# Kernel tuning notes

Measured on AMD Instinct MI355X. Metric: run time of the kernel, lower is better.

Reference implementation:

```python
import jax, jax.numpy as jnp
import numpy as np

B, S, D = 4, 4096, 1024  # batch, seq_len, input_dim == key_dim == value_dim == output_dim


def setup_inputs() -> dict:
    key = jax.random.key(0)
    kx, kq, kk, kv, kp = jax.random.split(key, 5)
    scale = 1.0 / np.sqrt(D)
    return {
        "x": jax.random.normal(kx, (B, S, D), dtype=jnp.float32),
        # weights stored as (in_dim, out_dim) so projection is x @ W
        "Wq": jax.random.normal(kq, (D, D), dtype=jnp.float32) * scale,
        "Wk": jax.random.normal(kk, (D, D), dtype=jnp.float32) * scale,
        "Wv": jax.random.normal(kv, (D, D), dtype=jnp.float32) * scale,
        "P": jax.random.normal(kp, (D, D), dtype=jnp.float32) * scale,
    }


def reference(x, Wq, Wk, Wv, P):
    # Linear (softmax-free) self-attention, faithful to the torch module:
    # Q K^T then (.)V, materializing the (B,S,S) score matrix as the original does.
    Q = jnp.einsum("bsd,dk->bsk", x, Wq)
    K = jnp.einsum("bsd,dk->bsk", x, Wk)
    V = jnp.einsum("bsd,dv->bsv", x, Wv)
    scores = jnp.einsum("bsk,btk->bst", Q, K)   # (B,S,S)
    context = jnp.einsum("bst,btv->bsv", scores, V)
    return x + jnp.einsum("bsv,vo->bso", context, P)
```

## Files before the change

### kernel.cpp

```cpp
#include <hip/hip_runtime.h>
#include <hip/hip_bf16.h>
#include <stdint.h>


#define BATCH 4
#define SEQ   4096
#define DIM   1024

#define TRI_SLICE 589824l

typedef __bf16 bf16x8 __attribute__((ext_vector_type(8)));
typedef float f32x4 __attribute__((ext_vector_type(4)));

static __device__ __forceinline__ unsigned short f2bf(float f) {
    unsigned int u = __builtin_bit_cast(unsigned int, f);
    u += 0x7fff + ((u >> 16) & 1);
    return (unsigned short)(u >> 16);
}
static __device__ __forceinline__ float bf2f(unsigned short h) {
    unsigned int u = (unsigned int)h << 16;
    return __builtin_bit_cast(float, u);
}

__global__ __launch_bounds__(256)
void gemm_fin(const unsigned short* __restrict__ Ag,
              const unsigned short* __restrict__ Btg,
              float* __restrict__ Cg,
              int K, int lda, int ldbt, int ldc,
              long sA, long sBt, long sC)
{
    __shared__ unsigned short As[3][128][32];
    __shared__ unsigned short Bs[3][256][32];

    const int gx = gridDim.x, gy = gridDim.y;
    const int nwg = gx * gy * gridDim.z;
    int id = blockIdx.x + gx * (blockIdx.y + gy * blockIdx.z);
    id = (id & 7) * (nwg >> 3) + (id >> 3);

    const int bx = id % gx;
    const int rest = id / gx;
    const int by = rest % gy;
    const int b = rest / gy;
    const long i0 = (long)by * 128;
    const long j0 = (long)bx * 256;

    const unsigned short* A  = Ag  + (long)b * sA;
    const unsigned short* Bt = Btg + (long)b * sBt;

    const int tid  = threadIdx.x;
    const int lane = tid & 63;
    const int w    = tid >> 6;
    const int wr   = w >> 1, wc = w & 1;
    const int srow = lane >> 2;
    const int sch  = lane & 3;
    const int fr   = lane & 15;
    const int kg   = lane >> 4;
    const int ch   = (kg ^ ((fr >> 1) & 3)) * 8;

    f32x4 acc[4][8] = {};
    const int nt = K / 32;

    auto stage = [&](int t, int buf) {
        const long kk = (long)t * 32;
        const long scoff = (long)((sch ^ ((srow >> 1) & 3)) * 8);
#pragma unroll
        for (int inst = 0; inst < 2; ++inst) {
            const int row = inst * 64 + w * 16 + srow;
            const unsigned short* src = A + (i0 + row) * lda + kk + scoff;
            __builtin_amdgcn_global_load_lds(
                (const __attribute__((address_space(1))) void*)src,
                (__attribute__((address_space(3))) void*)&As[buf][inst * 64 + w * 16][0],
                16, 0, 0);
        }
#pragma unroll
        for (int inst = 0; inst < 4; ++inst) {
            const int row = inst * 64 + w * 16 + srow;
            const unsigned short* src = Bt + (j0 + row) * ldbt + kk + scoff;
            __builtin_amdgcn_global_load_lds(
                (const __attribute__((address_space(1))) void*)src,
                (__attribute__((address_space(3))) void*)&Bs[buf][inst * 64 + w * 16][0],
                16, 0, 0);
        }
    };

    stage(0, 0);
    stage(1, 1);
    stage(2, 2);

    for (int t = 0; t < nt; ++t) {
        const int buf = t % 3;
        if (t < nt - 2)       asm volatile("s_waitcnt vmcnt(12)" ::: "memory");
        else if (t == nt - 2) asm volatile("s_waitcnt vmcnt(6)" ::: "memory");
        else                  asm volatile("s_waitcnt vmcnt(0)" ::: "memory");
        __builtin_amdgcn_s_barrier();
        asm volatile("" ::: "memory");

        bf16x8 af[4], bfv[8];
#pragma unroll
        for (int m = 0; m < 4; ++m)
            af[m] = *(const bf16x8*)&As[buf][wr * 64 + m * 16 + fr][ch];
#pragma unroll
        for (int n = 0; n < 8; ++n)
            bfv[n] = *(const bf16x8*)&Bs[buf][wc * 128 + n * 16 + fr][ch];

        asm volatile("s_waitcnt lgkmcnt(0)" ::: "memory");
        __builtin_amdgcn_sched_barrier(0);
        __builtin_amdgcn_s_barrier();
        asm volatile("" ::: "memory");

        if (t + 3 < nt) stage(t + 3, buf);
        __builtin_amdgcn_sched_barrier(0);

        __builtin_amdgcn_s_setprio(1);
#pragma unroll
        for (int m = 0; m < 4; ++m)
#pragma unroll
            for (int n = 0; n < 8; ++n)
                acc[m][n] = __builtin_amdgcn_mfma_f32_16x16x32_bf16(
                    af[m], bfv[n], acc[m][n], 0, 0, 0);
        __builtin_amdgcn_s_setprio(0);
    }

    float* C32 = Cg + (long)b * sC;
#pragma unroll
    for (int m = 0; m < 4; ++m) {
        const long rbase = i0 + wr * 64 + m * 16 + kg * 4;
#pragma unroll
        for (int n = 0; n < 8; ++n) {
            const long col = j0 + wc * 128 + n * 16 + fr;
#pragma unroll
            for (int q = 0; q < 4; ++q)
                C32[(rbase + q) * ldc + col] = acc[m][n][q];
        }
    }
}

template<int OUTMODE, int BN, bool TRI, bool ADD_I>
__global__ __launch_bounds__(256)
void gemm_db(const unsigned short* __restrict__ Ag,
             const unsigned short* __restrict__ Btg,
             void* __restrict__ Cg,
             int K, int zdiv, int lda, int ldbt, int ldc,
             long sA, long sBt, long sC)
{
    constexpr int NF = BN / 32;
    __shared__ unsigned short As[2][128][64];
    __shared__ unsigned short Bs[2][BN][64];

    const int gx = gridDim.x, gy = gridDim.y;
    const int nwg = gx * gy * gridDim.z;
    int id = blockIdx.x + gx * (blockIdx.y + gy * blockIdx.z);
    id = (id & 7) * (nwg >> 3) + (id >> 3);

    int z, tlin = 0;
    long i0, j0;
    if (TRI) {
        z = id / 36;
        tlin = id % 36;
        int t = tlin, ti = 0;
        while (t > ti) { t -= ti + 1; ++ti; }
        i0 = (long)ti * 128;
        j0 = (long)t * 128;
    } else {
        const int bx = id % gx;
        const int rest = id / gx;
        const int by = rest % gy;
        z = rest / gy;
        i0 = (long)by * 128;
        j0 = (long)bx * BN;
    }
    const int b = z / zdiv;
    const long koff = (long)(z % zdiv) * K;

    const unsigned short* A  = Ag  + (long)b * sA  + koff;
    const unsigned short* Bt = Btg + (long)b * sBt + koff;

    const int tid  = threadIdx.x;
    const int lane = tid & 63;
    const int w    = tid >> 6;
    const int wr   = w >> 1, wc = w & 1;
    const int lrow = lane >> 3;
    const int lcol = lane & 7;
    const int fr   = lane & 15;
    const int kg   = lane >> 4;
    const int scol = (lcol ^ lrow) * 8;

    f32x4 acc[4][NF] = {};

    const int nt = K / 64;

    auto stage = [&](int t, int buf) {
        const long kk = (long)t * 64;
#pragma unroll
        for (int inst = 0; inst < 4; ++inst) {
            const int row = w * 32 + inst * 8;
            const unsigned short* srcA = A + (i0 + row + lrow) * lda + kk + scol;
            __builtin_amdgcn_global_load_lds(
                (const __attribute__((address_space(1))) void*)srcA,
                (__attribute__((address_space(3))) void*)&As[buf][row][0], 16, 0, 0);
        }
#pragma unroll
        for (int inst = 0; inst < NF; ++inst) {
            const int row = w * (8 * NF) + inst * 8;
            const unsigned short* srcB = Bt + (j0 + row + lrow) * ldbt + kk + scol;
            __builtin_amdgcn_global_load_lds(
                (const __attribute__((address_space(1))) void*)srcB,
                (__attribute__((address_space(3))) void*)&Bs[buf][row][0], 16, 0, 0);
        }
    };

    stage(0, 0);
    stage(1, 1);

    for (int t = 0; t < nt; ++t) {
        const int buf = t & 1;
        if (t < nt - 1) {
            if constexpr (BN == 128)
                asm volatile("s_waitcnt vmcnt(8)" ::: "memory");
            else
                asm volatile("s_waitcnt vmcnt(6)" ::: "memory");
        } else {
            asm volatile("s_waitcnt vmcnt(0)" ::: "memory");
        }
        __builtin_amdgcn_s_barrier();
        asm volatile("" ::: "memory");

        bf16x8 af0[4], bf0[NF], af1[4], bf1[NF];
        const int ch0 = (kg ^ (fr & 7)) * 8;
        const int ch1 = ((4 + kg) ^ (fr & 7)) * 8;
#pragma unroll
        for (int m = 0; m < 4; ++m)
            af0[m] = *(const bf16x8*)&As[buf][wr * 64 + m * 16 + fr][ch0];
#pragma unroll
        for (int n = 0; n < NF; ++n)
            bf0[n] = *(const bf16x8*)&Bs[buf][wc * (BN / 2) + n * 16 + fr][ch0];
#pragma unroll
        for (int m = 0; m < 4; ++m)
            af1[m] = *(const bf16x8*)&As[buf][wr * 64 + m * 16 + fr][ch1];
#pragma unroll
        for (int n = 0; n < NF; ++n)
            bf1[n] = *(const bf16x8*)&Bs[buf][wc * (BN / 2) + n * 16 + fr][ch1];

        __builtin_amdgcn_s_setprio(1);
#pragma unroll
        for (int m = 0; m < 4; ++m)
#pragma unroll
            for (int n = 0; n < NF; ++n)
                acc[m][n] = __builtin_amdgcn_mfma_f32_16x16x32_bf16(
                    af0[m], bf0[n], acc[m][n], 0, 0, 0);
        __builtin_amdgcn_s_setprio(0);

        asm volatile("s_waitcnt lgkmcnt(0)" ::: "memory");
        __builtin_amdgcn_sched_barrier(0);
        __builtin_amdgcn_s_barrier();
        asm volatile("" ::: "memory");

        if (t + 2 < nt) stage(t + 2, buf);
        __builtin_amdgcn_sched_barrier(0);

        __builtin_amdgcn_s_setprio(1);
#pragma unroll
        for (int m = 0; m < 4; ++m)
#pragma unroll
            for (int n = 0; n < NF; ++n)
                acc[m][n] = __builtin_amdgcn_mfma_f32_16x16x32_bf16(
                    af1[m], bf1[n], acc[m][n], 0, 0, 0);
        __builtin_amdgcn_s_setprio(0);
    }

    if (OUTMODE == 3) {
        unsigned short* Cp = (unsigned short*)Cg + (long)z * TRI_SLICE
                           + (long)tlin * 16384;
#pragma unroll
        for (int m = 0; m < 4; ++m) {
            const int lrb = wr * 64 + m * 16 + kg * 4;
#pragma unroll
            for (int n = 0; n < NF; ++n) {
                const int lc = wc * (BN / 2) + n * 16 + fr;
#pragma unroll
                for (int q = 0; q < 4; ++q)
                    Cp[(lrb + q) * 128 + lc] = f2bf(acc[m][n][q]);
            }
        }
        return;
    }

    unsigned short* C16 = (OUTMODE == 1) ? ((unsigned short*)Cg + (long)b * sC) : nullptr;
    float*          C32 = (OUTMODE == 0) ? ((float*)Cg + (long)b * sC) : nullptr;
#pragma unroll
    for (int m = 0; m < 4; ++m) {
        const long rbase = i0 + wr * 64 + m * 16 + kg * 4;
#pragma unroll
        for (int n = 0; n < NF; ++n) {
            const long col = j0 + wc * (BN / 2) + n * 16 + fr;
#pragma unroll
            for (int q = 0; q < 4; ++q) {
                const long r = rbase + q;
                float v = acc[m][n][q];
                if (ADD_I && r == col) v += 1.0f;
                if (OUTMODE == 1) C16[r * ldc + col] = f2bf(v);
                else              C32[r * ldc + col] = v;
            }
        }
    }
}

__global__ __launch_bounds__(256)
void reduce_cast_tri(const unsigned short* __restrict__ part,
                     unsigned short* __restrict__ outG, int split)
{
    __shared__ unsigned short s[8][132];
    const long DD = (long)DIM * DIM;
    int id = blockIdx.x * 256 + threadIdx.x;
    const int b  = id / 147456;
    int rem      = id % 147456;
    const int tlin = rem / 4096;
    const int rr = rem % 4096;
    const int r  = rr >> 5;
    const int c4 = rr & 31;
    int t = tlin, ti = 0;
    while (t > ti) { t -= ti + 1; ++ti; }
    const long off = (long)tlin * 16384 + r * 128 + c4 * 4;

    float4 sum = make_float4(0.f, 0.f, 0.f, 0.f);
    for (int sp = 0; sp < split; ++sp) {
        ushort4 v = *(const ushort4*)&part[(long)(b * split + sp) * TRI_SLICE + off];
        sum.x += bf2f(v.x); sum.y += bf2f(v.y); sum.z += bf2f(v.z); sum.w += bf2f(v.w);
    }
    ushort4 o;
    o.x = f2bf(sum.x); o.y = f2bf(sum.y); o.z = f2bf(sum.z); o.w = f2bf(sum.w);
    *(ushort4*)&outG[b * DD + ((long)ti * 128 + r) * DIM + (long)t * 128 + c4 * 4] = o;

    if (t == ti) return;

    const int rl = r & 7;
    s[rl][c4 * 4 + 0] = o.x; s[rl][c4 * 4 + 1] = o.y;
    s[rl][c4 * 4 + 2] = o.z; s[rl][c4 * 4 + 3] = o.w;
    __syncthreads();

    const int r0 = r & ~7;
    const int co = threadIdx.x >> 1;
    const int hf = threadIdx.x & 1;
    ushort4 m;
    m.x = s[hf * 4 + 0][co]; m.y = s[hf * 4 + 1][co];
    m.z = s[hf * 4 + 2][co]; m.w = s[hf * 4 + 3][co];
    *(ushort4*)&outG[b * DD + ((long)t * 128 + co) * DIM
                     + (long)ti * 128 + r0 + hf * 4] = m;
}

__global__ __launch_bounds__(256)
void prep_all(const float* __restrict__ x,
              const float* __restrict__ Wq, const float* __restrict__ Wk,
              const float* __restrict__ Wv, const float* __restrict__ P,
              unsigned short* __restrict__ xb, unsigned short* __restrict__ xTb,
              unsigned short* __restrict__ Wqb, unsigned short* __restrict__ Wkb,
              unsigned short* __restrict__ Wvb, unsigned short* __restrict__ Ptb)
{
    __shared__ unsigned short t[32][33];
    const int z = blockIdx.z;
    const int row = threadIdx.x >> 3;
    const int cid = threadIdx.x & 7;

    if (z < BATCH) {
        const long base = (long)z * SEQ * DIM;
        const int r0 = blockIdx.y * 32;
        const int c0 = blockIdx.x * 32;
        float4 v = *(const float4*)&x[base + (long)(r0 + row) * DIM + c0 + cid * 4];
        ushort4 h;
        h.x = f2bf(v.x); h.y = f2bf(v.y); h.z = f2bf(v.z); h.w = f2bf(v.w);
        *(ushort4*)&xb[base + (long)(r0 + row) * DIM + c0 + cid * 4] = h;
        t[row][cid * 4 + 0] = h.x; t[row][cid * 4 + 1] = h.y;
        t[row][cid * 4 + 2] = h.z; t[row][cid * 4 + 3] = h.w;
        __syncthreads();
        ushort4 o;
        o.x = t[cid * 4 + 0][row];
        o.y = t[cid * 4 + 1][row];
        o.z = t[cid * 4 + 2][row];
        o.w = t[cid * 4 + 3][row];
        *(ushort4*)&xTb[base + (long)(c0 + row) * SEQ + r0 + cid * 4] = o;
        return;
    }

    const int wsel = blockIdx.y >> 5;
    const int r0 = (blockIdx.y & 31) * 32;
    const int c0 = blockIdx.x * 32;
    const float* src = (wsel == 0) ? Wq : (wsel == 1) ? Wk : (wsel == 2) ? Wv : P;
    float4 v = *(const float4*)&src[(long)(r0 + row) * DIM + c0 + cid * 4];
    ushort4 h;
    h.x = f2bf(v.x); h.y = f2bf(v.y); h.z = f2bf(v.z); h.w = f2bf(v.w);

    if (wsel < 3) {
        unsigned short* dst = (wsel == 0) ? Wqb : (wsel == 1) ? Wkb : Wvb;
        *(ushort4*)&dst[(long)(r0 + row) * DIM + c0 + cid * 4] = h;
        return;
    }
    t[row][cid * 4 + 0] = h.x; t[row][cid * 4 + 1] = h.y;
    t[row][cid * 4 + 2] = h.z; t[row][cid * 4 + 3] = h.w;
    __syncthreads();
    ushort4 o;
    o.x = t[cid * 4 + 0][row];
    o.y = t[cid * 4 + 1][row];
    o.z = t[cid * 4 + 2][row];
    o.w = t[cid * 4 + 3][row];
    *(ushort4*)&Ptb[(long)(c0 + row) * DIM + r0 + cid * 4] = o;
}

extern "C" void kernel_launch(void* const* d_in, const int* in_sizes, int n_in,
                              void* d_out, int out_size, void* d_ws, size_t ws_size,
                              hipStream_t stream)
{
    const float* x  = (const float*)d_in[0];
    const float* Wq = (const float*)d_in[1];
    const float* Wk = (const float*)d_in[2];
    const float* Wv = (const float*)d_in[3];
    const float* P  = (const float*)d_in[4];
    float* out = (float*)d_out;

    const long DD = (long)DIM * DIM;
    const long SD = (long)SEQ * DIM;

    uint8_t* ws = (uint8_t*)d_ws;
    unsigned short* xb   = (unsigned short*)(ws);
    unsigned short* xTb  = (unsigned short*)(ws + (32ul << 20));
    unsigned short* Hb   = (unsigned short*)(ws + (32ul << 20));
    unsigned short* Ntb  = (unsigned short*)(ws + (40ul << 20));
    unsigned short* Gb   = (unsigned short*)(ws + (64ul << 20));
    unsigned short* Wqb  = (unsigned short*)(ws + (72ul << 20));
    unsigned short* Ptb  = (unsigned short*)(ws + (74ul << 20));
    unsigned short* Wkb  = (unsigned short*)(ws + (76ul << 20));
    unsigned short* Wvb  = (unsigned short*)(ws + (78ul << 20));
    unsigned short* Ub   = (unsigned short*)(ws + (80ul << 20));
    unsigned short* W2Tb = (unsigned short*)(ws + (82ul << 20));
    unsigned short* regA = (unsigned short*)(ws + (84ul << 20));

    const int split = 8;

    prep_all<<<dim3(DIM / 32, SEQ / 32, BATCH + 1), 256, 0, stream>>>(
        x, Wq, Wk, Wv, P, xb, xTb, Wqb, Wkb, Wvb, Ptb);

    gemm_db<3, 128, true, false><<<dim3(36 * split * BATCH, 1, 1), 256, 0, stream>>>(
        xTb, xTb, regA, SEQ / split, split, SEQ, SEQ, DIM, SD, SD, 0);
    reduce_cast_tri<<<dim3(BATCH * 36 * 128 * 32 / 256), 256, 0, stream>>>(
        regA, Gb, split);

    gemm_db<1, 64, false, false><<<dim3(16, 8, 2), 256, 0, stream>>>(
        Wqb, Wkb, Ub, DIM, 1, DIM, DIM, DIM, DD, DD, DD);

    gemm_db<1, 64, false, false><<<dim3(16, 8, BATCH), 256, 0, stream>>>(
        Ub, Gb, Hb, DIM, 1, DIM, DIM, DIM, 0, DD, DD);

    gemm_db<1, 64, false, true><<<dim3(16, 8, BATCH), 256, 0, stream>>>(
        W2Tb, Hb, Ntb, DIM, 1, DIM, DIM, DIM, 0, DD, DD);

    gemm_fin<<<dim3(DIM / 256, SEQ / 128, BATCH), 256, 0, stream>>>(
        xb, Ntb, out, DIM, DIM, DIM, DIM, SD, DD, SD);
}
```

Baseline: 165.0 us.

## Load B fragments directly from global into registers, bypassing LDS staging

In the fp32-output GEMM, the B operand is no longer staged through a triple-buffered LDS tile. Each wave now loads its B fragments straight from global memory into registers every k-step, and only A stays in LDS. Synchronisation is restructured around this, and launch bounds now request two workgroups per CU. The aim is to cut LDS footprint and LDS traffic to raise occupancy. In exchange, B rows are read twice from global/L2, since they are no longer shared across the two wave rows. The B loads are also issued just before use without prefetching, so their latency may be exposed.

```diff
diff --git a/kernel.cpp b/kernel.cpp
--- a/kernel.cpp
+++ b/kernel.cpp
@@ -22,7 +22,7 @@
     return __builtin_bit_cast(float, u);
 }
 
-__global__ __launch_bounds__(256)
+__global__ __launch_bounds__(256, 2)
 void gemm_fin(const unsigned short* __restrict__ Ag,
               const unsigned short* __restrict__ Btg,
               float* __restrict__ Cg,
@@ -30,7 +30,6 @@
               long sA, long sBt, long sC)
 {
     __shared__ unsigned short As[3][128][32];
-    __shared__ unsigned short Bs[3][256][32];
 
     const int gx = gridDim.x, gy = gridDim.y;
     const int nwg = gx * gy * gridDim.z;
@@ -57,10 +56,15 @@
     const int kg   = lane >> 4;
     const int ch   = (kg ^ ((fr >> 1) & 3)) * 8;
 
+    const unsigned short* Brow[8];
+#pragma unroll
+    for (int n = 0; n < 8; ++n)
+        Brow[n] = Bt + (j0 + wc * 128 + n * 16 + fr) * (long)ldbt + kg * 8;
+
     f32x4 acc[4][8] = {};
     const int nt = K / 32;
 
-    auto stage = [&](int t, int buf) {
+    auto stageA = [&](int t, int buf) {
         const long kk = (long)t * 32;
         const long scoff = (long)((sch ^ ((srow >> 1) & 3)) * 8);
 #pragma unroll
@@ -72,43 +76,35 @@
                 (__attribute__((address_space(3))) void*)&As[buf][inst * 64 + w * 16][0],
                 16, 0, 0);
         }
-#pragma unroll
-        for (int inst = 0; inst < 4; ++inst) {
-            const int row = inst * 64 + w * 16 + srow;
-            const unsigned short* src = Bt + (j0 + row) * ldbt + kk + scoff;
-            __builtin_amdgcn_global_load_lds(
-                (const __attribute__((address_space(1))) void*)src,
-                (__attribute__((address_space(3))) void*)&Bs[buf][inst * 64 + w * 16][0],
-                16, 0, 0);
-        }
     };
 
-    stage(0, 0);
-    stage(1, 1);
-    stage(2, 2);
+    stageA(0, 0);
+    stageA(1, 1);
+    stageA(2, 2);
+    asm volatile("s_waitcnt vmcnt(4)" ::: "memory");
+    __builtin_amdgcn_s_barrier();
+    asm volatile("" ::: "memory");
 
     for (int t = 0; t < nt; ++t) {
         const int buf = t % 3;
-        if (t < nt - 2)       asm volatile("s_waitcnt vmcnt(12)" ::: "memory");
-        else if (t == nt - 2) asm volatile("s_waitcnt vmcnt(6)" ::: "memory");
-        else                  asm volatile("s_waitcnt vmcnt(0)" ::: "memory");
-        __builtin_amdgcn_s_barrier();
-        asm volatile("" ::: "memory");
-
-        bf16x8 af[4], bfv[8];
+        const long kk = (long)t * 32;
+
+        bf16x8 bv[8];
+#pragma unroll
+        for (int n = 0; n < 8; ++n)
+            bv[n] = *(const bf16x8*)&Brow[n][kk];
+
+        bf16x8 af[4];
 #pragma unroll
         for (int m = 0; m < 4; ++m)
             af[m] = *(const bf16x8*)&As[buf][wr * 64 + m * 16 + fr][ch];
-#pragma unroll
-        for (int n = 0; n < 8; ++n)
-            bfv[n] = *(const bf16x8*)&Bs[buf][wc * 128 + n * 16 + fr][ch];
 
         asm volatile("s_waitcnt lgkmcnt(0)" ::: "memory");
         __builtin_amdgcn_sched_barrier(0);
         __builtin_amdgcn_s_barrier();
         asm volatile("" ::: "memory");
 
-        if (t + 3 < nt) stage(t + 3, buf);
+        if (t + 3 < nt) stageA(t + 3, buf);
         __builtin_amdgcn_sched_barrier(0);
 
         __builtin_amdgcn_s_setprio(1);
@@ -117,8 +113,11 @@
 #pragma unroll
             for (int n = 0; n < 8; ++n)
                 acc[m][n] = __builtin_amdgcn_mfma_f32_16x16x32_bf16(
-                    af[m], bfv[n], acc[m][n], 0, 0, 0);
+                    af[m], bv[n], acc[m][n], 0, 0, 0);
         __builtin_amdgcn_s_setprio(0);
+
+        __builtin_amdgcn_s_barrier();
+        asm volatile("" ::: "memory");
     }
 
     float* C32 = Cg + (long)b * sC;
```

After: 198.8 us. +20.5%, slower.

## Enlarge final GEMM tile to 256x256 with 512 threads and K=64 double buffering

Applied to the files above, without the earlier changes.

The final x·N GEMM moves from a 128x256 tile with 256 threads, K=32 steps and triple buffering to a 256x256 tile with 8 waves, K=64 steps and double buffering, using a new XOR swizzle. Each K step is split into two MFMA halves so LDS reads for the second half overlap the first half's math. The aim is more operand reuse per tile and fewer barriers per FLOP. In exchange, LDS per block rises to 128KB and the grid shrinks to 256 blocks, which may reduce occupancy and latency hiding.

```diff
diff --git a/kernel.cpp b/kernel.cpp
--- a/kernel.cpp
+++ b/kernel.cpp
@@ -22,15 +22,15 @@
     return __builtin_bit_cast(float, u);
 }
 
-__global__ __launch_bounds__(256)
-void gemm_fin(const unsigned short* __restrict__ Ag,
-              const unsigned short* __restrict__ Btg,
-              float* __restrict__ Cg,
-              int K, int lda, int ldbt, int ldc,
-              long sA, long sBt, long sC)
+__global__ __launch_bounds__(512)
+void gemm_db256(const unsigned short* __restrict__ Ag,
+                const unsigned short* __restrict__ Btg,
+                float* __restrict__ Cg,
+                int K, int lda, int ldbt, int ldc,
+                long sA, long sBt, long sC)
 {
-    __shared__ unsigned short As[3][128][32];
-    __shared__ unsigned short Bs[3][256][32];
+    __shared__ unsigned short As[2][256][64];
+    __shared__ unsigned short Bs[2][256][64];
 
     const int gx = gridDim.x, gy = gridDim.y;
     const int nwg = gx * gy * gridDim.z;
@@ -41,7 +41,7 @@
     const int rest = id / gx;
     const int by = rest % gy;
     const int b = rest / gy;
-    const long i0 = (long)by * 128;
+    const long i0 = (long)by * 256;
     const long j0 = (long)bx * 256;
 
     const unsigned short* A  = Ag  + (long)b * sA;
@@ -50,84 +50,95 @@
     const int tid  = threadIdx.x;
     const int lane = tid & 63;
     const int w    = tid >> 6;
-    const int wr   = w >> 1, wc = w & 1;
-    const int srow = lane >> 2;
-    const int sch  = lane & 3;
+    const int wr   = w >> 2;
+    const int wc   = w & 3;
+    const int lrow = lane >> 3;
+    const int lcol = lane & 7;
     const int fr   = lane & 15;
     const int kg   = lane >> 4;
-    const int ch   = (kg ^ ((fr >> 1) & 3)) * 8;
-
-    f32x4 acc[4][8] = {};
-    const int nt = K / 32;
+    const int scol = (lcol ^ lrow) * 8;
+
+    f32x4 acc[8][4] = {};
+
+    const int nt = K / 64;
 
     auto stage = [&](int t, int buf) {
-        const long kk = (long)t * 32;
-        const long scoff = (long)((sch ^ ((srow >> 1) & 3)) * 8);
-#pragma unroll
-        for (int inst = 0; inst < 2; ++inst) {
-            const int row = inst * 64 + w * 16 + srow;
-            const unsigned short* src = A + (i0 + row) * lda + kk + scoff;
+        const long kk = (long)t * 64;
+#pragma unroll
+        for (int inst = 0; inst < 4; ++inst) {
+            const int row = w * 32 + inst * 8;
+            const unsigned short* srcA = A + (i0 + row + lrow) * lda + kk + scol;
             __builtin_amdgcn_global_load_lds(
-                (const __attribute__((address_space(1))) void*)src,
-                (__attribute__((address_space(3))) void*)&As[buf][inst * 64 + w * 16][0],
-                16, 0, 0);
-        }
-#pragma unroll
-        for (int inst = 0; inst < 4; ++inst) {
-            const int row = inst * 64 + w * 16 + srow;
-            const unsigned short* src = Bt + (j0 + row) * ldbt + kk + scoff;
+                (const __attribute__((address_space(1))) void*)srcA,
+                (__attribute__((address_space(3))) void*)&As[buf][row][0], 16, 0, 0);
+            const unsigned short* srcB = Bt + (j0 + row + lrow) * ldbt + kk + scol;
             __builtin_amdgcn_global_load_lds(
-                (const __attribute__((address_space(1))) void*)src,
-                (__attribute__((address_space(3))) void*)&Bs[buf][inst * 64 + w * 16][0],
-                16, 0, 0);
+                (const __attribute__((address_space(1))) void*)srcB,
+                (__attribute__((address_space(3))) void*)&Bs[buf][row][0], 16, 0, 0);
         }
     };
 
     stage(0, 0);
     stage(1, 1);
-    stage(2, 2);
 
     for (int t = 0; t < nt; ++t) {
-        const int buf = t % 3;
-        if (t < nt - 2)       asm volatile("s_waitcnt vmcnt(12)" ::: "memory");
-        else if (t == nt - 2) asm volatile("s_waitcnt vmcnt(6)" ::: "memory");
-        else                  asm volatile("s_waitcnt vmcnt(0)" ::: "memory");
+        const int buf = t & 1;
+        if (t < nt - 1) asm volatile("s_waitcnt vmcnt(8)" ::: "memory");
+        else            asm volatile("s_waitcnt vmcnt(0)" ::: "memory");
         __builtin_amdgcn_s_barrier();
         asm volatile("" ::: "memory");
 
-        bf16x8 af[4], bfv[8];
-#pragma unroll
-        for (int m = 0; m < 4; ++m)
-            af[m] = *(const bf16x8*)&As[buf][wr * 64 + m * 16 + fr][ch];
-#pragma unroll
-        for (int n = 0; n < 8; ++n)
-            bfv[n] = *(const bf16x8*)&Bs[buf][wc * 128 + n * 16 + fr][ch];
+        const int ch0 = (kg ^ (fr & 7)) * 8;
+        bf16x8 af0[8], bf0[4];
+#pragma unroll
+        for (int m = 0; m < 8; ++m)
+            af0[m] = *(const bf16x8*)&As[buf][wr * 128 + m * 16 + fr][ch0];
+#pragma unroll
+        for (int n = 0; n < 4; ++n)
+            bf0[n] = *(const bf16x8*)&Bs[buf][wc * 64 + n * 16 + fr][ch0];
+        __builtin_amdgcn_s_setprio(1);
+#pragma unroll
+        for (int m = 0; m < 8; ++m)
+#pragma unroll
+            for (int n = 0; n < 4; ++n)
+                acc[m][n] = __builtin_amdgcn_mfma_f32_16x16x32_bf16(
+                    af0[m], bf0[n], acc[m][n], 0, 0, 0);
+        __builtin_amdgcn_s_setprio(0);
+
+        const int ch1 = ((4 + kg) ^ (fr & 7)) * 8;
+        bf16x8 af1[8], bf1[4];
+#pragma unroll
+        for (int m = 0; m < 8; ++m)
+            af1[m] = *(const bf16x8*)&As[buf][wr * 128 + m * 16 + fr][ch1];
+#pragma unroll
+        for (int n = 0; n < 4; ++n)
+            bf1[n] = *(const bf16x8*)&Bs[buf][wc * 64 + n * 16 + fr][ch1];
 
         asm volatile("s_waitcnt lgkmcnt(0)" ::: "memory");
         __builtin_amdgcn_sched_barrier(0);
         __builtin_amdgcn_s_barrier();
         asm volatile("" ::: "memory");
 
-        if (t + 3 < nt) stage(t + 3, buf);
+        if (t + 2 < nt) stage(t + 2, buf);
         __builtin_amdgcn_sched_barrier(0);
 
         __builtin_amdgcn_s_setprio(1);
 #pragma unroll
-        for (int m = 0; m < 4; ++m)
-#pragma unroll
-            for (int n = 0; n < 8; ++n)
+        for (int m = 0; m < 8; ++m)
+#pragma unroll
+            for (int n = 0; n < 4; ++n)
                 acc[m][n] = __builtin_amdgcn_mfma_f32_16x16x32_bf16(
-                    af[m], bfv[n], acc[m][n], 0, 0, 0);
+                    af1[m], bf1[n], acc[m][n], 0, 0, 0);
         __builtin_amdgcn_s_setprio(0);
     }
 
     float* C32 = Cg + (long)b * sC;
 #pragma unroll
-    for (int m = 0; m < 4; ++m) {
-        const long rbase = i0 + wr * 64 + m * 16 + kg * 4;
-#pragma unroll
-        for (int n = 0; n < 8; ++n) {
-            const long col = j0 + wc * 128 + n * 16 + fr;
+    for (int m = 0; m < 8; ++m) {
+        const long rbase = i0 + wr * 128 + m * 16 + kg * 4;
+#pragma unroll
+        for (int n = 0; n < 4; ++n) {
+            const long col = j0 + wc * 64 + n * 16 + fr;
 #pragma unroll
             for (int q = 0; q < 4; ++q)
                 C32[(rbase + q) * ldc + col] = acc[m][n][q];
@@ -452,6 +463,6 @@
     gemm_db<1, 64, false, true><<<dim3(16, 8, BATCH), 256, 0, stream>>>(
         W2Tb, Hb, Ntb, DIM, 1, DIM, DIM, DIM, 0, DD, DD);
 
-    gemm_fin<<<dim3(DIM / 256, SEQ / 128, BATCH), 256, 0, stream>>>(
+    gemm_db256<<<dim3(DIM / 256, SEQ / 256, BATCH), 512, 0, stream>>>(
         xb, Ntb, out, DIM, DIM, DIM, DIM, SD, DD, SD);
 }
```

Measured after the change: 163.3 us. About the same (-1.0%).
